# Performance work log

Hardware: AMD Instinct MI355X
Metric: run time of the kernel (lower is better)

Reference implementation:

```python
import jax, jax.numpy as jnp
import numpy as np

N_NODES = 100000


def gcn_conv(x, edge_index, W, b):
    # PyG GCNConv: add self-loops, symmetric normalization, then scatter-add.
    n = x.shape[0]
    loops = jnp.arange(n, dtype=edge_index.dtype)
    src = jnp.concatenate([edge_index[0], loops])
    dst = jnp.concatenate([edge_index[1], loops])
    h = x @ W  # [N, F_out] -- transform before propagate (small GEMM)
    ones = jnp.ones(src.shape[0], dtype=x.dtype)
    deg = jax.ops.segment_sum(ones, dst, num_segments=n)  # in-degree incl. self-loop
    dinv = jnp.where(deg > 0, jax.lax.rsqrt(deg), 0.0)
    norm = dinv[src] * dinv[dst]  # [E+N]
    msg = h[src] * norm[:, None]  # gather + scale, [E+N, F_out]
    out = jax.ops.segment_sum(msg, dst, num_segments=n)  # scatter-add
    return out + b


def setup_inputs() -> dict:
    key = jax.random.key(0)
    k1, k2, k3, k4 = jax.random.split(key, 4)
    d = 128
    x = jax.random.normal(k1, (N_NODES, d), dtype=jnp.float32)
    edge_index = jax.random.randint(k2, (2, 1600000), 0, N_NODES, dtype=jnp.int64)
    scale = 1.0 / np.sqrt(d)
    W1 = jax.random.normal(k3, (d, d), dtype=jnp.float32) * scale
    b1 = jnp.zeros((d,), dtype=jnp.float32)
    W2 = jax.random.normal(k4, (d, d), dtype=jnp.float32) * scale
    b2 = jnp.zeros((d,), dtype=jnp.float32)
    return {"x": x, "edge_index": edge_index, "W1": W1, "b1": b1, "W2": W2, "b2": b2}


def reference(x, edge_index, W1, b1, W2, b2):
    # Layer 1: GCNConv -> relu -> dropout(eval: identity)
    h = jax.nn.relu(gcn_conv(x, edge_index, W1, b1))
    # Layer 2
    h = jax.nn.relu(gcn_conv(h, edge_index, W2, b2))
    return h
```

## Files before the change

kernel.cpp:

```cpp
#include <hip/hip_runtime.h>


#define NFEAT 128
#define BSH 7
#define MAXNB 1024
#define BCAP 4096
#define BPITCH 136
#define EPITCH 132

typedef __attribute__((ext_vector_type(8))) short s8v;
typedef __attribute__((ext_vector_type(4))) float f4v;
typedef __attribute__((ext_vector_type(2))) float f2v;
typedef __attribute__((ext_vector_type(4))) uint u4v;

__device__ inline ushort f2bf(float f) {
    union { float f; uint u; } x; x.f = f;
    uint u = x.u;
    return (ushort)((u + 0x7fffu + ((u >> 16) & 1u)) >> 16);
}
__device__ inline f2v unpk(uint u) {
    union { uint u; float f; } lo, hi;
    lo.u = u << 16;
    hi.u = u & 0xffff0000u;
    return (f2v){lo.f, hi.f};
}
__device__ inline void upfma2(uint4 v, float g, f2v* a) {
    a[0] += g * unpk(v.x);
    a[1] += g * unpk(v.y);
    a[2] += g * unpk(v.z);
    a[3] += g * unpk(v.w);
}

template <bool ABF16>
__device__ inline void gemm_body(ushort* Bs, int bid, const void* __restrict__ Ap,
                                 const float* __restrict__ W,
                                 ushort* __restrict__ hs, int M) {
    int t = threadIdx.x;

#pragma unroll
    for (int i = 0; i < 16; i++) {
        int idx = t + i * 256;
        int k4 = idx >> 7;
        int n = idx & 127;
        ushort o[4];
#pragma unroll
        for (int j = 0; j < 4; j++) o[j] = f2bf(W[(k4 * 4 + j) * NFEAT + n]);
        uint2 pk;
        __builtin_memcpy(&pk, o, 8);
        *(uint2*)&Bs[n * BPITCH + k4 * 4] = pk;
    }
    __syncthreads();

    int w = t >> 6, l = t & 63;
    int q = l >> 4, ln = l & 15;
    int wid = bid * 4 + w;
    int row0 = wid * 32;
    bool alive = row0 < M;
    if (!alive) row0 = (M - 32) & ~31;

    s8v afr[2][4];
#pragma unroll
    for (int mt = 0; mt < 2; mt++) {
        int row = row0 + mt * 16 + ln;
        if (row >= M) row = M - 1;
        if (ABF16) {
            const ushort* A = (const ushort*)Ap + (size_t)row * NFEAT + q * 8;
#pragma unroll
            for (int ks = 0; ks < 4; ks++)
                afr[mt][ks] = *(const s8v*)(A + ks * 32);
        } else {
            const float* A = (const float*)Ap + (size_t)row * NFEAT + q * 8;
#pragma unroll
            for (int ks = 0; ks < 4; ks++) {
                float4 f0 = *(const float4*)(A + ks * 32);
                float4 f1 = *(const float4*)(A + ks * 32 + 4);
                ushort o[8] = {f2bf(f0.x), f2bf(f0.y), f2bf(f0.z), f2bf(f0.w),
                               f2bf(f1.x), f2bf(f1.y), f2bf(f1.z), f2bf(f1.w)};
                __builtin_memcpy(&afr[mt][ks], o, 16);
            }
        }
    }

    f4v acc[2][8];
#pragma unroll
    for (int mt = 0; mt < 2; mt++)
#pragma unroll
        for (int nt = 0; nt < 8; nt++) acc[mt][nt] = (f4v){0.f, 0.f, 0.f, 0.f};
#pragma unroll
    for (int nt = 0; nt < 8; nt++) {
        const ushort* Bp = Bs + (nt * 16 + ln) * BPITCH + q * 8;
#pragma unroll
        for (int ks = 0; ks < 4; ks++) {
            s8v bfr = *(const s8v*)(Bp + ks * 32);
            acc[0][nt] = __builtin_amdgcn_mfma_f32_16x16x32_bf16(afr[0][ks], bfr, acc[0][nt], 0, 0, 0);
            acc[1][nt] = __builtin_amdgcn_mfma_f32_16x16x32_bf16(afr[1][ks], bfr, acc[1][nt], 0, 0, 0);
        }
    }
    __syncthreads();

    ushort* ow = Bs + w * 32 * EPITCH;
#pragma unroll
    for (int mt = 0; mt < 2; mt++) {
#pragma unroll
        for (int r = 0; r < 4; r++) {
            int lrow = mt * 16 + q * 4 + r;
#pragma unroll
            for (int nt = 0; nt < 8; nt++)
                ow[lrow * EPITCH + nt * 16 + ln] = f2bf(acc[mt][nt][r]);
        }
    }
    __builtin_amdgcn_s_waitcnt(0);
#pragma unroll
    for (int i = 0; i < 8; i++) {
        int idx = l + i * 64;
        int r = idx >> 4, c = idx & 15;
        const ushort* p = ow + r * EPITCH + c * 8;
        uint2 lo = *(const uint2*)p;
        uint2 hi = *(const uint2*)(p + 4);
        uint4 v = make_uint4(lo.x, lo.y, hi.x, hi.y);
        if (alive) *(uint4*)(hs + (size_t)(row0 + r) * NFEAT + c * 8) = v;
    }
}

__global__ __launch_bounds__(256) void k_fused1(const int* __restrict__ src,
                                                const int* __restrict__ dst,
                                                int* __restrict__ gcnt,
                                                uint* __restrict__ ebuf,
                                                int E, int NB, int CH, int chBlk,
                                                const float* __restrict__ x,
                                                const float* __restrict__ W1,
                                                ushort* __restrict__ hs, int M) {
    __shared__ __align__(16) ushort smem[128 * BPITCH];
    if (blockIdx.x < chBlk) {
        int* h = (int*)smem;
        int t = threadIdx.x;
        for (int i = t; i < NB; i += 256) h[i] = 0;
        __syncthreads();
        int e0 = blockIdx.x * CH;
        int e1 = min(e0 + CH, E);
        for (int e = e0 + t; e < e1; e += 256) atomicAdd(&h[dst[e] >> BSH], 1);
        __syncthreads();
        for (int i = t; i < NB; i += 256) {
            int c = h[i];
            h[i] = c ? (i * BCAP + atomicAdd(&gcnt[i], c)) : 0;
        }
        __syncthreads();
        for (int e = e0 + t; e < e1; e += 256) {
            int d = dst[e];
            int b = d >> BSH;
            int p = atomicAdd(&h[b], 1);
            if (p < (b + 1) * BCAP)
                ebuf[p] = ((uint)src[e] << BSH) | (uint)(d & ((1 << BSH) - 1));
        }
    } else {
        gemm_body<false>(smem, blockIdx.x - chBlk, x, W1, hs, M);
    }
}

template <bool ABF16>
__global__ __launch_bounds__(256) void k_gemm3(const void* __restrict__ Ap,
                                               const float* __restrict__ W,
                                               ushort* __restrict__ hs, int M) {
    __shared__ __align__(16) ushort Bs[128 * BPITCH];
    gemm_body<ABF16>(Bs, blockIdx.x, Ap, W, hs, M);
}

__global__ __launch_bounds__(256) void k_fill2(const uint* __restrict__ ebuf,
                                               const int* __restrict__ gcnt,
                                               int* __restrict__ row_ptr,
                                               float* __restrict__ dinv,
                                               int* __restrict__ col,
                                               int N, int E, int NB) {
    __shared__ int cnt[128];
    __shared__ int pre[128];
    __shared__ int sred[256];
    __shared__ int colL[BCAP];
    int b = blockIdx.x;
    int t = threadIdx.x;
    int part = 0;
    for (int j = t; j < b; j += 256) part += gcnt[j];
    sred[t] = part;
    __syncthreads();
    for (int off = 128; off >= 1; off >>= 1) {
        if (t < off) sred[t] += sred[t + off];
        __syncthreads();
    }
    int gb = sred[0];
    int m = min(gcnt[b], BCAP);
    if (t < 128) cnt[t] = 0;
    __syncthreads();
    const uint* eb = ebuf + (size_t)b * BCAP;
    for (int i = t; i < m; i += 256) atomicAdd(&cnt[eb[i] & 127], 1);
    __syncthreads();
    if (t < 128) pre[t] = cnt[t];
    __syncthreads();
    for (int off = 1; off < 128; off <<= 1) {
        int add = (t >= off && t < 128) ? pre[t - off] : 0;
        __syncthreads();
        if (t < 128) pre[t] += add;
        __syncthreads();
    }
    if (t < 128) {
        pre[t] -= cnt[t];
        int node = (b << BSH) + t;
        if (node < N) {
            row_ptr[node] = gb + pre[t];
            dinv[node] = rsqrtf((float)(cnt[t] + 1));
        }
    }
    __syncthreads();
    for (int i = t; i < m; i += 256) {
        uint p = eb[i];
        int pos = atomicAdd(&pre[p & 127], 1);
        colL[pos] = (int)(p >> BSH);
    }
    __syncthreads();
    for (int i = t; i < m; i += 256) col[gb + i] = colL[i];
    if (b == NB - 1 && t == 0) row_ptr[N] = E;
}

template <bool OUT_BF16>
__global__ __launch_bounds__(256) void k_aggregate(const uint4* __restrict__ hs4,
                                                   const int* __restrict__ row_ptr,
                                                   const int* __restrict__ col,
                                                   const float* __restrict__ dinv,
                                                   const float* __restrict__ bias,
                                                   void* __restrict__ outp, int N) {
    int node = blockIdx.x * 16 + (threadIdx.x >> 4);
    if (node >= N) return;
    int sub = threadIdx.x & 15;

    uint4 vself = hs4[(size_t)node * 16 + sub];
    float dself = dinv[node];
    int s = row_ptr[node], e = row_ptr[node + 1];
    int nb = (e - s) >> 2;

    f2v a[4];
#pragma unroll
    for (int j = 0; j < 4; j++) a[j] = (f2v){0.f, 0.f};

    int k = s;
    if (nb > 0) {
        int c0 = col[k], c1 = col[k + 1], c2 = col[k + 2], c3 = col[k + 3];
        uint4 v0 = hs4[(size_t)c0 * 16 + sub];
        uint4 v1 = hs4[(size_t)c1 * 16 + sub];
        uint4 v2 = hs4[(size_t)c2 * 16 + sub];
        uint4 v3 = hs4[(size_t)c3 * 16 + sub];
        float g0 = dinv[c0], g1 = dinv[c1], g2 = dinv[c2], g3 = dinv[c3];
        int d0 = col[k + 4], d1 = col[k + 5], d2 = col[k + 6], d3 = col[k + 7];
        k += 8;
        upfma2(vself, dself, a);
        for (int it = 1; it < nb; ++it, k += 4) {
            uint4 w0 = hs4[(size_t)d0 * 16 + sub];
            uint4 w1 = hs4[(size_t)d1 * 16 + sub];
            uint4 w2 = hs4[(size_t)d2 * 16 + sub];
            uint4 w3 = hs4[(size_t)d3 * 16 + sub];
            float h0 = dinv[d0], h1 = dinv[d1], h2 = dinv[d2], h3 = dinv[d3];
            int t0 = col[k], t1 = col[k + 1], t2 = col[k + 2], t3 = col[k + 3];
            upfma2(v0, g0, a); upfma2(v1, g1, a); upfma2(v2, g2, a); upfma2(v3, g3, a);
            v0 = w0; v1 = w1; v2 = w2; v3 = w3;
            g0 = h0; g1 = h1; g2 = h2; g3 = h3;
            d0 = t0; d1 = t1; d2 = t2; d3 = t3;
        }
        upfma2(v0, g0, a); upfma2(v1, g1, a); upfma2(v2, g2, a); upfma2(v3, g3, a);
        k = s + nb * 4;
    } else {
        upfma2(vself, dself, a);
    }
    for (; k < e; ++k) {
        int c = col[k];
        upfma2(hs4[(size_t)c * 16 + sub], dinv[c], a);
    }

    float di = dinv[node];
    const float4* b4 = (const float4*)bias;
    float4 b0 = b4[sub * 2], b1 = b4[sub * 2 + 1];
    float r[8];
    r[0] = fmaxf(fmaf(di, a[0].x, b0.x), 0.f);
    r[1] = fmaxf(fmaf(di, a[0].y, b0.y), 0.f);
    r[2] = fmaxf(fmaf(di, a[1].x, b0.z), 0.f);
    r[3] = fmaxf(fmaf(di, a[1].y, b0.w), 0.f);
    r[4] = fmaxf(fmaf(di, a[2].x, b1.x), 0.f);
    r[5] = fmaxf(fmaf(di, a[2].y, b1.y), 0.f);
    r[6] = fmaxf(fmaf(di, a[3].x, b1.z), 0.f);
    r[7] = fmaxf(fmaf(di, a[3].y, b1.w), 0.f);
    if (OUT_BF16) {
        ushort o[8];
#pragma unroll
        for (int j = 0; j < 8; j++) o[j] = f2bf(r[j]);
        u4v pk;
        __builtin_memcpy(&pk, o, 16);
        __builtin_nontemporal_store(pk, (u4v*)outp + (size_t)node * 16 + sub);
    } else {
        float* orow = (float*)outp + (size_t)node * NFEAT + sub * 8;
        f4v r0 = {r[0], r[1], r[2], r[3]};
        f4v r1 = {r[4], r[5], r[6], r[7]};
        __builtin_nontemporal_store(r0, (f4v*)orow);
        __builtin_nontemporal_store(r1, (f4v*)(orow + 4));
    }
}

extern "C" void kernel_launch(void* const* d_in, const int* in_sizes, int n_in,
                              void* d_out, int out_size, void* d_ws, size_t ws_size,
                              hipStream_t stream) {
    const float* x = (const float*)d_in[0];
    const int* ei = (const int*)d_in[1];
    const float* W1 = (const float*)d_in[2];
    const float* b1 = (const float*)d_in[3];
    const float* W2 = (const float*)d_in[4];
    const float* b2 = (const float*)d_in[5];
    float* out = (float*)d_out;

    const int N = in_sizes[0] / NFEAT;
    const int E = in_sizes[1] / 2;
    const int* src = ei;
    const int* dst = ei + E;
    const int NB = (N + (1 << BSH) - 1) >> BSH;

    char* w = (char*)d_ws;
    size_t off = 0;
    auto alloc = [&](size_t bytes) -> void* {
        void* p = w + off;
        off = (off + bytes + 511) & ~(size_t)511;
        return p;
    };
    ushort* hs = (ushort*)alloc((size_t)N * NFEAT * 2);
    ushort* y1 = (ushort*)alloc((size_t)N * NFEAT * 2);
    int* row_ptr = (int*)alloc((size_t)(N + 1) * 4);
    float* dinv = (float*)alloc((size_t)N * 4);
    int* col = (int*)alloc((size_t)E * 4);
    uint* ebuf = (uint*)alloc((size_t)NB * BCAP * 4);
    int* gcnt = (int*)alloc((size_t)MAXNB * 4);
    (void)ws_size; (void)n_in; (void)out_size;

    const int CH = 2048;
    const int chBlk = (E + CH - 1) / CH;
    const int gemmBlk = (N + 127) / 128;
    const int aggBlk = (N + 15) / 16;

    hipMemsetAsync(gcnt, 0, (size_t)MAXNB * 4, stream);
    k_fused1<<<chBlk + gemmBlk, 256, 0, stream>>>(src, dst, gcnt, ebuf, E, NB, CH, chBlk,
                                                  x, W1, hs, N);
    k_fill2<<<NB, 256, 0, stream>>>(ebuf, gcnt, row_ptr, dinv, col, N, E, NB);

    k_aggregate<true><<<aggBlk, 256, 0, stream>>>((const uint4*)hs, row_ptr, col, dinv, b1, y1, N);
    k_gemm3<true><<<gemmBlk, 256, 0, stream>>>(y1, W2, hs, N);
    k_aggregate<false><<<aggBlk, 256, 0, stream>>>((const uint4*)hs, row_ptr, col, dinv, b2, out, N);
}
```

Before: 320.9 us.

## Replace bucketed CSR build with global atomic degree count, scan, and scatter

Swaps the two-level bucket sort (per-chunk shared histograms into fixed-capacity buckets, then per-bucket local sort) for a plain CSR build: global atomic degree count, a two-pass block scan to get row_ptr and dinv, then an atomic scatter of src indices into col. The first GEMM is no longer fused with the edge binning and runs as its own launch. This removes the capped bucket buffer and the block-local sort, but adds more launches and many global atomics on random destinations. Neighbour order within a row also becomes nondeterministic, which can hurt gather locality in the aggregation.

```diff
diff --git a/kernel.cpp b/kernel.cpp
--- a/kernel.cpp
+++ b/kernel.cpp
@@ -2,9 +2,6 @@
 
 
 #define NFEAT 128
-#define BSH 7
-#define MAXNB 1024
-#define BCAP 4096
 #define BPITCH 136
 #define EPITCH 132
 
@@ -31,10 +28,101 @@
     a[3] += g * unpk(v.w);
 }
 
+__global__ __launch_bounds__(256) void k_deg(const int* __restrict__ dst,
+                                             int* __restrict__ deg, int E) {
+    int i = blockIdx.x * 256 + threadIdx.x;
+    int stride = gridDim.x * 256;
+    int E4 = E >> 2;
+    const int4* d4 = (const int4*)dst;
+    for (int k = i; k < E4; k += stride) {
+        int4 v = d4[k];
+        atomicAdd(&deg[v.x], 1);
+        atomicAdd(&deg[v.y], 1);
+        atomicAdd(&deg[v.z], 1);
+        atomicAdd(&deg[v.w], 1);
+    }
+    for (int k = E4 * 4 + i; k < E; k += stride) atomicAdd(&deg[dst[k]], 1);
+}
+
+__global__ __launch_bounds__(256) void k_scan_a(const int* __restrict__ deg,
+                                                int* __restrict__ bsum, int N) {
+    __shared__ int red[256];
+    int t = threadIdx.x;
+    int n = blockIdx.x * 256 + t;
+    red[t] = (n < N) ? deg[n] : 0;
+    __syncthreads();
+    for (int off = 128; off >= 1; off >>= 1) {
+        if (t < off) red[t] += red[t + off];
+        __syncthreads();
+    }
+    if (t == 0) bsum[blockIdx.x] = red[0];
+}
+
+__global__ __launch_bounds__(256) void k_scan_b(const int* __restrict__ deg,
+                                                const int* __restrict__ bsum,
+                                                int* __restrict__ row_ptr,
+                                                int* __restrict__ wofs,
+                                                float* __restrict__ dinv,
+                                                int N, int E) {
+    __shared__ int red[256];
+    __shared__ int sc[256];
+    int b = blockIdx.x, t = threadIdx.x;
+    int part = 0;
+    for (int j = t; j < b; j += 256) part += bsum[j];
+    red[t] = part;
+    __syncthreads();
+    for (int off = 128; off >= 1; off >>= 1) {
+        if (t < off) red[t] += red[t + off];
+        __syncthreads();
+    }
+    int base = red[0];
+    int n = b * 256 + t;
+    int d = (n < N) ? deg[n] : 0;
+    sc[t] = d;
+    __syncthreads();
+    for (int off = 1; off < 256; off <<= 1) {
+        int add = (t >= off) ? sc[t - off] : 0;
+        __syncthreads();
+        sc[t] += add;
+        __syncthreads();
+    }
+    if (n < N) {
+        int excl = base + sc[t] - d;
+        row_ptr[n] = excl;
+        wofs[n] = excl;
+        dinv[n] = rsqrtf((float)(d + 1));
+    }
+    if (n == N - 1) row_ptr[N] = E;
+}
+
+__global__ __launch_bounds__(256) void k_scat(const int* __restrict__ src,
+                                              const int* __restrict__ dst,
+                                              int* __restrict__ wofs,
+                                              int* __restrict__ col, int E) {
+    int i = blockIdx.x * 256 + threadIdx.x;
+    int stride = gridDim.x * 256;
+    int E4 = E >> 2;
+    const int4* s4 = (const int4*)src;
+    const int4* d4 = (const int4*)dst;
+    for (int k = i; k < E4; k += stride) {
+        int4 d = d4[k];
+        int4 s = s4[k];
+        col[atomicAdd(&wofs[d.x], 1)] = s.x;
+        col[atomicAdd(&wofs[d.y], 1)] = s.y;
+        col[atomicAdd(&wofs[d.z], 1)] = s.z;
+        col[atomicAdd(&wofs[d.w], 1)] = s.w;
+    }
+    for (int k = E4 * 4 + i; k < E; k += stride) {
+        int p = atomicAdd(&wofs[dst[k]], 1);
+        col[p] = src[k];
+    }
+}
+
 template <bool ABF16>
-__device__ inline void gemm_body(ushort* Bs, int bid, const void* __restrict__ Ap,
-                                 const float* __restrict__ W,
-                                 ushort* __restrict__ hs, int M) {
+__global__ __launch_bounds__(256) void k_gemm3(const void* __restrict__ Ap,
+                                               const float* __restrict__ W,
+                                               ushort* __restrict__ hs, int M) {
+    __shared__ __align__(16) ushort Bs[128 * BPITCH];
     int t = threadIdx.x;
 
 #pragma unroll
@@ -53,7 +141,7 @@
 
     int w = t >> 6, l = t & 63;
     int q = l >> 4, ln = l & 15;
-    int wid = bid * 4 + w;
+    int wid = blockIdx.x * 4 + w;
     int row0 = wid * 32;
     bool alive = row0 < M;
     if (!alive) row0 = (M - 32) & ~31;
@@ -120,103 +208,6 @@
         uint4 v = make_uint4(lo.x, lo.y, hi.x, hi.y);
         if (alive) *(uint4*)(hs + (size_t)(row0 + r) * NFEAT + c * 8) = v;
     }
-}
-
-__global__ __launch_bounds__(256) void k_fused1(const int* __restrict__ src,
-                                                const int* __restrict__ dst,
-                                                int* __restrict__ gcnt,
-                                                uint* __restrict__ ebuf,
-                                                int E, int NB, int CH, int chBlk,
-                                                const float* __restrict__ x,
-                                                const float* __restrict__ W1,
-                                                ushort* __restrict__ hs, int M) {
-    __shared__ __align__(16) ushort smem[128 * BPITCH];
-    if (blockIdx.x < chBlk) {
-        int* h = (int*)smem;
-        int t = threadIdx.x;
-        for (int i = t; i < NB; i += 256) h[i] = 0;
-        __syncthreads();
-        int e0 = blockIdx.x * CH;
-        int e1 = min(e0 + CH, E);
-        for (int e = e0 + t; e < e1; e += 256) atomicAdd(&h[dst[e] >> BSH], 1);
-        __syncthreads();
-        for (int i = t; i < NB; i += 256) {
-            int c = h[i];
-            h[i] = c ? (i * BCAP + atomicAdd(&gcnt[i], c)) : 0;
-        }
-        __syncthreads();
-        for (int e = e0 + t; e < e1; e += 256) {
-            int d = dst[e];
-            int b = d >> BSH;
-            int p = atomicAdd(&h[b], 1);
-            if (p < (b + 1) * BCAP)
-                ebuf[p] = ((uint)src[e] << BSH) | (uint)(d & ((1 << BSH) - 1));
-        }
-    } else {
-        gemm_body<false>(smem, blockIdx.x - chBlk, x, W1, hs, M);
-    }
-}
-
-template <bool ABF16>
-__global__ __launch_bounds__(256) void k_gemm3(const void* __restrict__ Ap,
-                                               const float* __restrict__ W,
-                                               ushort* __restrict__ hs, int M) {
-    __shared__ __align__(16) ushort Bs[128 * BPITCH];
-    gemm_body<ABF16>(Bs, blockIdx.x, Ap, W, hs, M);
-}
-
-__global__ __launch_bounds__(256) void k_fill2(const uint* __restrict__ ebuf,
-                                               const int* __restrict__ gcnt,
-                                               int* __restrict__ row_ptr,
-                                               float* __restrict__ dinv,
-                                               int* __restrict__ col,
-                                               int N, int E, int NB) {
-    __shared__ int cnt[128];
-    __shared__ int pre[128];
-    __shared__ int sred[256];
-    __shared__ int colL[BCAP];
-    int b = blockIdx.x;
-    int t = threadIdx.x;
-    int part = 0;
-    for (int j = t; j < b; j += 256) part += gcnt[j];
-    sred[t] = part;
-    __syncthreads();
-    for (int off = 128; off >= 1; off >>= 1) {
-        if (t < off) sred[t] += sred[t + off];
-        __syncthreads();
-    }
-    int gb = sred[0];
-    int m = min(gcnt[b], BCAP);
-    if (t < 128) cnt[t] = 0;
-    __syncthreads();
-    const uint* eb = ebuf + (size_t)b * BCAP;
-    for (int i = t; i < m; i += 256) atomicAdd(&cnt[eb[i] & 127], 1);
-    __syncthreads();
-    if (t < 128) pre[t] = cnt[t];
-    __syncthreads();
-    for (int off = 1; off < 128; off <<= 1) {
-        int add = (t >= off && t < 128) ? pre[t - off] : 0;
-        __syncthreads();
-        if (t < 128) pre[t] += add;
-        __syncthreads();
-    }
-    if (t < 128) {
-        pre[t] -= cnt[t];
-        int node = (b << BSH) + t;
-        if (node < N) {
-            row_ptr[node] = gb + pre[t];
-            dinv[node] = rsqrtf((float)(cnt[t] + 1));
-        }
-    }
-    __syncthreads();
-    for (int i = t; i < m; i += 256) {
-        uint p = eb[i];
-        int pos = atomicAdd(&pre[p & 127], 1);
-        colL[pos] = (int)(p >> BSH);
-    }
-    __syncthreads();
-    for (int i = t; i < m; i += 256) col[gb + i] = colL[i];
-    if (b == NB - 1 && t == 0) row_ptr[N] = E;
 }
 
 template <bool OUT_BF16>
@@ -315,7 +306,7 @@
     const int E = in_sizes[1] / 2;
     const int* src = ei;
     const int* dst = ei + E;
-    const int NB = (N + (1 << BSH) - 1) >> BSH;
+    const int NSB = (N + 255) / 256;
 
     char* w = (char*)d_ws;
     size_t off = 0;
@@ -327,22 +318,24 @@
     ushort* hs = (ushort*)alloc((size_t)N * NFEAT * 2);
     ushort* y1 = (ushort*)alloc((size_t)N * NFEAT * 2);
     int* row_ptr = (int*)alloc((size_t)(N + 1) * 4);
+    int* col = (int*)alloc((size_t)(E + 64) * 4);
     float* dinv = (float*)alloc((size_t)N * 4);
-    int* col = (int*)alloc((size_t)E * 4);
-    uint* ebuf = (uint*)alloc((size_t)NB * BCAP * 4);
-    int* gcnt = (int*)alloc((size_t)MAXNB * 4);
+    int* deg = (int*)alloc((size_t)N * 4);
+    int* wofs = (int*)alloc((size_t)N * 4);
+    int* bsum = (int*)alloc((size_t)NSB * 4);
     (void)ws_size; (void)n_in; (void)out_size;
 
-    const int CH = 2048;
-    const int chBlk = (E + CH - 1) / CH;
     const int gemmBlk = (N + 127) / 128;
     const int aggBlk = (N + 15) / 16;
-
-    hipMemsetAsync(gcnt, 0, (size_t)MAXNB * 4, stream);
-    k_fused1<<<chBlk + gemmBlk, 256, 0, stream>>>(src, dst, gcnt, ebuf, E, NB, CH, chBlk,
-                                                  x, W1, hs, N);
-    k_fill2<<<NB, 256, 0, stream>>>(ebuf, gcnt, row_ptr, dinv, col, N, E, NB);
-
+    const int edgeBlk = 1536;
+
+    hipMemsetAsync(deg, 0, (size_t)N * 4, stream);
+    k_deg<<<edgeBlk, 256, 0, stream>>>(dst, deg, E);
+    k_scan_a<<<NSB, 256, 0, stream>>>(deg, bsum, N);
+    k_scan_b<<<NSB, 256, 0, stream>>>(deg, bsum, row_ptr, wofs, dinv, N, E);
+    k_scat<<<edgeBlk, 256, 0, stream>>>(src, dst, wofs, col, E);
+
+    k_gemm3<false><<<gemmBlk, 256, 0, stream>>>(x, W1, hs, N);
     k_aggregate<true><<<aggBlk, 256, 0, stream>>>((const uint4*)hs, row_ptr, col, dinv, b1, y1, N);
     k_gemm3<true><<<gemmBlk, 256, 0, stream>>>(y1, W2, hs, N);
     k_aggregate<false><<<aggBlk, 256, 0, stream>>>((const uint4*)hs, row_ptr, col, dinv, b2, out, N);
```

New measurement: 458.6 us. +42.9%, slower.

## Shrink GEMM tiles, stage W in K-halves, interleave scatter and GEMM blocks

Applied to the files above, without the earlier changes.

The GEMM body now gives each wave 16 rows instead of 32 and loads W into shared memory in two 64-wide K halves with a smaller pitch. It writes results straight to global memory, dropping the LDS epilogue transpose. This cuts LDS use and raises occupancy, and the grid doubles to N/64 blocks. The fused first kernel also interleaves edge-bucketing blocks with GEMM blocks (one scatter per three blocks) so both workloads run concurrently rather than back to back. The cost is redundant W conversion per block, an extra sync, and uncoalesced 2-byte global stores.

```diff
diff --git a/kernel.cpp b/kernel.cpp
--- a/kernel.cpp
+++ b/kernel.cpp
@@ -5,8 +5,7 @@
 #define BSH 7
 #define MAXNB 1024
 #define BCAP 4096
-#define BPITCH 136
-#define EPITCH 132
+#define HP 72
 
 typedef __attribute__((ext_vector_type(8))) short s8v;
 typedef __attribute__((ext_vector_type(4))) float f4v;
@@ -36,89 +35,68 @@
                                  const float* __restrict__ W,
                                  ushort* __restrict__ hs, int M) {
     int t = threadIdx.x;
-
-#pragma unroll
-    for (int i = 0; i < 16; i++) {
-        int idx = t + i * 256;
-        int k4 = idx >> 7;
-        int n = idx & 127;
-        ushort o[4];
-#pragma unroll
-        for (int j = 0; j < 4; j++) o[j] = f2bf(W[(k4 * 4 + j) * NFEAT + n]);
-        uint2 pk;
-        __builtin_memcpy(&pk, o, 8);
-        *(uint2*)&Bs[n * BPITCH + k4 * 4] = pk;
-    }
-    __syncthreads();
-
     int w = t >> 6, l = t & 63;
     int q = l >> 4, ln = l & 15;
-    int wid = bid * 4 + w;
-    int row0 = wid * 32;
-    bool alive = row0 < M;
-    if (!alive) row0 = (M - 32) & ~31;
-
-    s8v afr[2][4];
-#pragma unroll
-    for (int mt = 0; mt < 2; mt++) {
-        int row = row0 + mt * 16 + ln;
-        if (row >= M) row = M - 1;
-        if (ABF16) {
-            const ushort* A = (const ushort*)Ap + (size_t)row * NFEAT + q * 8;
-#pragma unroll
-            for (int ks = 0; ks < 4; ks++)
-                afr[mt][ks] = *(const s8v*)(A + ks * 32);
-        } else {
-            const float* A = (const float*)Ap + (size_t)row * NFEAT + q * 8;
-#pragma unroll
-            for (int ks = 0; ks < 4; ks++) {
-                float4 f0 = *(const float4*)(A + ks * 32);
-                float4 f1 = *(const float4*)(A + ks * 32 + 4);
-                ushort o[8] = {f2bf(f0.x), f2bf(f0.y), f2bf(f0.z), f2bf(f0.w),
-                               f2bf(f1.x), f2bf(f1.y), f2bf(f1.z), f2bf(f1.w)};
-                __builtin_memcpy(&afr[mt][ks], o, 16);
+    int row0 = (bid * 4 + w) * 16;
+
+    int arow = row0 + ln;
+    if (arow >= M) arow = M - 1;
+    s8v afr[4];
+    if (ABF16) {
+        const ushort* A = (const ushort*)Ap + (size_t)arow * NFEAT + q * 8;
+#pragma unroll
+        for (int g = 0; g < 4; g++) afr[g] = *(const s8v*)(A + g * 32);
+    } else {
+        const float* A = (const float*)Ap + (size_t)arow * NFEAT + q * 8;
+#pragma unroll
+        for (int g = 0; g < 4; g++) {
+            float4 f0 = *(const float4*)(A + g * 32);
+            float4 f1 = *(const float4*)(A + g * 32 + 4);
+            ushort o[8] = {f2bf(f0.x), f2bf(f0.y), f2bf(f0.z), f2bf(f0.w),
+                           f2bf(f1.x), f2bf(f1.y), f2bf(f1.z), f2bf(f1.w)};
+            __builtin_memcpy(&afr[g], o, 16);
+        }
+    }
+
+    f4v acc[8];
+#pragma unroll
+    for (int nt = 0; nt < 8; nt++) acc[nt] = (f4v){0.f, 0.f, 0.f, 0.f};
+
+#pragma unroll
+    for (int h = 0; h < 2; h++) {
+        if (h) __syncthreads();
+#pragma unroll
+        for (int i = 0; i < 8; i++) {
+            int idx = t + i * 256;
+            int k4 = idx >> 7;
+            int n = idx & 127;
+            ushort o[4];
+#pragma unroll
+            for (int j = 0; j < 4; j++) o[j] = f2bf(W[(h * 64 + k4 * 4 + j) * NFEAT + n]);
+            uint2 pk;
+            __builtin_memcpy(&pk, o, 8);
+            *(uint2*)&Bs[n * HP + k4 * 4] = pk;
+        }
+        __syncthreads();
+#pragma unroll
+        for (int nt = 0; nt < 8; nt++) {
+            const ushort* Bp = Bs + (nt * 16 + ln) * HP + q * 8;
+#pragma unroll
+            for (int ks = 0; ks < 2; ks++) {
+                s8v bfr = *(const s8v*)(Bp + ks * 32);
+                acc[nt] = __builtin_amdgcn_mfma_f32_16x16x32_bf16(afr[h * 2 + ks], bfr, acc[nt], 0, 0, 0);
             }
         }
     }
 
-    f4v acc[2][8];
-#pragma unroll
-    for (int mt = 0; mt < 2; mt++)
-#pragma unroll
-        for (int nt = 0; nt < 8; nt++) acc[mt][nt] = (f4v){0.f, 0.f, 0.f, 0.f};
-#pragma unroll
-    for (int nt = 0; nt < 8; nt++) {
-        const ushort* Bp = Bs + (nt * 16 + ln) * BPITCH + q * 8;
-#pragma unroll
-        for (int ks = 0; ks < 4; ks++) {
-            s8v bfr = *(const s8v*)(Bp + ks * 32);
-            acc[0][nt] = __builtin_amdgcn_mfma_f32_16x16x32_bf16(afr[0][ks], bfr, acc[0][nt], 0, 0, 0);
-            acc[1][nt] = __builtin_amdgcn_mfma_f32_16x16x32_bf16(afr[1][ks], bfr, acc[1][nt], 0, 0, 0);
-        }
-    }
-    __syncthreads();
-
-    ushort* ow = Bs + w * 32 * EPITCH;
-#pragma unroll
-    for (int mt = 0; mt < 2; mt++) {
-#pragma unroll
-        for (int r = 0; r < 4; r++) {
-            int lrow = mt * 16 + q * 4 + r;
-#pragma unroll
-            for (int nt = 0; nt < 8; nt++)
-                ow[lrow * EPITCH + nt * 16 + ln] = f2bf(acc[mt][nt][r]);
-        }
-    }
-    __builtin_amdgcn_s_waitcnt(0);
-#pragma unroll
-    for (int i = 0; i < 8; i++) {
-        int idx = l + i * 64;
-        int r = idx >> 4, c = idx & 15;
-        const ushort* p = ow + r * EPITCH + c * 8;
-        uint2 lo = *(const uint2*)p;
-        uint2 hi = *(const uint2*)(p + 4);
-        uint4 v = make_uint4(lo.x, lo.y, hi.x, hi.y);
-        if (alive) *(uint4*)(hs + (size_t)(row0 + r) * NFEAT + c * 8) = v;
+#pragma unroll
+    for (int r = 0; r < 4; r++) {
+        int row = row0 + q * 4 + r;
+        if (row < M) {
+            ushort* hp = hs + (size_t)row * NFEAT + ln;
+#pragma unroll
+            for (int nt = 0; nt < 8; nt++) hp[nt * 16] = f2bf(acc[nt][r]);
+        }
     }
 }
 
@@ -130,13 +108,15 @@
                                                 const float* __restrict__ x,
                                                 const float* __restrict__ W1,
                                                 ushort* __restrict__ hs, int M) {
-    __shared__ __align__(16) ushort smem[128 * BPITCH];
-    if (blockIdx.x < chBlk) {
+    __shared__ __align__(16) ushort smem[128 * HP];
+    int bid = blockIdx.x;
+    int sid = bid / 3, r = bid % 3;
+    if (r == 0 && sid < chBlk) {
         int* h = (int*)smem;
         int t = threadIdx.x;
         for (int i = t; i < NB; i += 256) h[i] = 0;
         __syncthreads();
-        int e0 = blockIdx.x * CH;
+        int e0 = sid * CH;
         int e1 = min(e0 + CH, E);
         for (int e = e0 + t; e < e1; e += 256) atomicAdd(&h[dst[e] >> BSH], 1);
         __syncthreads();
@@ -153,7 +133,8 @@
                 ebuf[p] = ((uint)src[e] << BSH) | (uint)(d & ((1 << BSH) - 1));
         }
     } else {
-        gemm_body<false>(smem, blockIdx.x - chBlk, x, W1, hs, M);
+        int scats_before = min(sid + (r ? 1 : 0), chBlk);
+        gemm_body<false>(smem, bid - scats_before, x, W1, hs, M);
     }
 }
 
@@ -161,7 +142,7 @@
 __global__ __launch_bounds__(256) void k_gemm3(const void* __restrict__ Ap,
                                                const float* __restrict__ W,
                                                ushort* __restrict__ hs, int M) {
-    __shared__ __align__(16) ushort Bs[128 * BPITCH];
+    __shared__ __align__(16) ushort Bs[128 * HP];
     gemm_body<ABF16>(Bs, blockIdx.x, Ap, W, hs, M);
 }
 
@@ -328,14 +309,14 @@
     ushort* y1 = (ushort*)alloc((size_t)N * NFEAT * 2);
     int* row_ptr = (int*)alloc((size_t)(N + 1) * 4);
     float* dinv = (float*)alloc((size_t)N * 4);
-    int* col = (int*)alloc((size_t)E * 4);
+    int* col = (int*)alloc((size_t)(E + 64) * 4);
     uint* ebuf = (uint*)alloc((size_t)NB * BCAP * 4);
     int* gcnt = (int*)alloc((size_t)MAXNB * 4);
     (void)ws_size; (void)n_in; (void)out_size;
 
     const int CH = 2048;
     const int chBlk = (E + CH - 1) / CH;
-    const int gemmBlk = (N + 127) / 128;
+    const int gemmBlk = (N + 63) / 64;
     const int aggBlk = (N + 15) / 16;
 
     hipMemsetAsync(gcnt, 0, (size_t)MAXNB * 4, stream);
```

Measured after the change: 306.1 us. 1.05x faster.
